# Kernel tuning notes

Measured on AMD Instinct MI355X. Metric: run time of the kernel, lower is better.

## Reference

```python
import jax, jax.numpy as jnp
import numpy as np

DIM = 100
SAMPLE_DS = 0.5
MAX_S = int(DIM / SAMPLE_DS) + 1  # 201, matches torch sample_ds_arr
DIRECTIONS = ['x', 'x', 'y', 'y']  # constant in the original forward


def _polygon_area(poly):
    # poly: [bs, num_v, 2]; shoelace-style area identical to torch loop
    y_max = jnp.max(poly[:, :, 1], axis=-1)            # [bs]
    x0 = poly[:, :, 0]; y0 = poly[:, :, 1]
    x1 = jnp.roll(x0, -1, axis=1); y1 = jnp.roll(y0, -1, axis=1)
    s = jnp.sum((x1 - x0) * (y_max[:, None] - (y1 + y0) * 0.5), axis=1)
    return jnp.abs(s)


def _line_sum(mask_m, x0, x1, y0, y1, axis_x):
    # mask_m: [bs, DIM, DIM]; x0,x1,y0,y1: [bs, num_v]
    # Vectorized version of torch get_samples + interpolated_sum:
    # masked_select/dedup are replaced by boolean keep masks (samples along an
    # edge are monotone, so the valid set is a contiguous run and "previous
    # compacted sample" == "previous step").
    steps = jnp.arange(MAX_S, dtype=mask_m.dtype)      # [S]
    vx = x1 - x0 + 1e-6
    vy = y1 - y0 + 1e-6
    n = jnp.sqrt(vx * vx + vy * vy)
    vx = vx / n; vy = vy / n
    xs = x0[..., None] + steps * vx[..., None]         # [bs, nv, S]
    ys = y0[..., None] + steps * vy[..., None]
    xlo = jnp.minimum(x0, x1)[..., None]; xhi = jnp.maximum(x0, x1)[..., None]
    ylo = jnp.minimum(y0, y1)[..., None]; yhi = jnp.maximum(y0, y1)[..., None]
    seg = ((xs <= xhi + 1e-3) & (xs >= xlo - 1e-3) &
           (ys <= yhi + 1e-3) & (ys >= ylo - 1e-3))
    u = xs if axis_x else ys
    bound = (u <= DIM - 1) & (u >= 0.0)
    valid = seg & bound
    # dedup on floor(u) along sample axis (torch get_uniques)
    fu = jnp.floor(u)
    prev_valid = jnp.pad(valid[..., :-1], ((0, 0), (0, 0), (1, 0)))
    prev_fu = jnp.pad(fu[..., :-1], ((0, 0), (0, 0), (1, 0)))
    first = valid & ~prev_valid
    keep = valid & (first | (fu != prev_fu))
    # bilinear interpolation (torch interpolated_sum)
    X0f = jnp.floor(xs); Y0f = jnp.floor(ys)
    w00 = (X0f + 1 - xs) * (Y0f + 1 - ys)
    w01 = (X0f + 1 - xs) * (ys - Y0f)
    w10 = (xs - X0f) * (Y0f + 1 - ys)
    w11 = (xs - X0f) * (ys - Y0f)
    Xi0 = jnp.clip(X0f, 0, DIM - 1).astype(jnp.int32)
    Xi1 = jnp.clip(X0f + 1, 0, DIM - 1).astype(jnp.int32)
    Yi0 = jnp.clip(Y0f, 0, DIM - 1).astype(jnp.int32)
    Yi1 = jnp.clip(Y0f + 1, 0, DIM - 1).astype(jnp.int32)
    gather = jax.vmap(lambda m, yy, xx: m[yy, xx])      # over batch
    val = (w00 * gather(mask_m, Yi0, Xi0) + w01 * gather(mask_m, Yi1, Xi0) +
           w10 * gather(mask_m, Yi0, Xi1) + w11 * gather(mask_m, Yi1, Xi1))
    return jnp.sum(jnp.where(keep, val, 0.0), axis=-1)  # [bs, nv]


def _polygon_area_mask(poly, gt_mask):
    # poly: [bs, nv, 2], gt_mask: [bs, 4, DIM, DIM]
    x0 = poly[:, :, 0]; y0 = poly[:, :, 1]
    x1 = jnp.roll(x0, -1, axis=1); y1 = jnp.roll(y0, -1, axis=1)
    ret = jnp.zeros(poly.shape[0], dtype=poly.dtype)
    for m, d in enumerate(DIRECTIONS):
        ax = (d == 'x')
        sign = jnp.where((x1 > x0) if ax else (y1 > y0), 1.0, -1.0)
        sf = _line_sum(gt_mask[:, m], x0, x1, y0, y1, ax)
        sb = _line_sum(gt_mask[:, m], x1, x0, y1, y0, ax)
        s = jnp.sum(sign * (sf + sb) * 0.5, axis=1)
        ret = ret + jnp.abs(s)
    return ret / len(DIRECTIONS)


def setup_inputs() -> dict:
    key = jax.random.key(0)
    k1, k2, k3 = jax.random.split(key, 3)
    bs, nv = 512, 64
    poly = jax.random.uniform(k1, (bs, nv, 2), dtype=jnp.float32) * (DIM - 1)
    gt = jax.random.uniform(k2, (bs, nv, 2), dtype=jnp.float32) * (DIM - 1)
    gt_mask = jax.random.uniform(k3, (bs, 4, DIM, DIM), dtype=jnp.float32)
    return {"poly": poly, "gt": gt, "gt_mask": gt_mask}


def reference(poly, gt, gt_mask):
    pred_area = _polygon_area(poly)
    gt_area = _polygon_area(gt)
    int_area = _polygon_area_mask(poly, gt_mask)
    union_area = pred_area + gt_area - int_area
    return int_area / union_area
```

## Files before the change

### kernel.cpp

```cpp
#include <hip/hip_runtime.h>
#include <math.h>

#define DIM   100
#define NV    64
#define BS    512
#define MAXCH 1792

template<bool AX>
__device__ __forceinline__ float mainloop(
    const unsigned char* smask, const float (*prm)[8],
    const unsigned short* chunkTab, int totE, int tid) {
  const int grp = tid >> 5;
  const int sub = (tid >> 3) & 3;
  const int st  = tid & 7;
  const int base0 = grp * 16 + sub * 4;
  float acc = 0.0f;

  for (int i = 0; i * 128 < totE; ++i) {
    const ushort4 ent = *reinterpret_cast<const ushort4*>(
        &chunkTab[i * 128 + base0]);

    #define SAMPLE(e) {                                                    \
      const int c = (e) >> 4;                                              \
      const float kf = (float)((((e) & 15) << 3) | st);                    \
      const float4 p = *reinterpret_cast<const float4*>(&prm[c][0]);       \
      const float4 q = *reinterpret_cast<const float4*>(&prm[c][4]);       \
      const float vu = AX ? p.z : p.w;                                     \
      const float u0 = AX ? p.x : p.y;                                     \
      const float fu0 = floorf(u0);                                        \
      const float ck = fu0 + ((vu > 0.0f) ? kf : -kf);                     \
      const float te = ceilf(fmaf(kf, q.z, q.w) - 0.005f);                 \
      const float u1 = __fadd_rn(__fmul_rn(te, vu), u0);                   \
      float t = (floorf(u1) == ck) ? te : (te + 1.0f);                     \
      t = fminf(fmaxf(t, 0.0f), 300.0f);                                   \
      const float xs = __fadd_rn(__fmul_rn(t, p.z), p.x);                  \
      const float ys = __fadd_rn(__fmul_rn(t, p.w), p.y);                  \
      const float X0 = floorf(xs), Y0 = floorf(ys);                        \
      const float wx1 = xs - X0, wy1 = ys - Y0;                            \
      const float wx0 = 1.0f - wx1, wy0 = 1.0f - wy1;                      \
      const int ix0 = (int)X0, iy0 = (int)Y0;                              \
      const int xi0 = min(max(ix0, 0), DIM - 1);                           \
      const int xi1 = min(max(ix0 + 1, 0), DIM - 1);                       \
      const int yi0 = min(max(iy0, 0), DIM - 1);                           \
      const int yi1 = min(max(iy0 + 1, 0), DIM - 1);                       \
      const int a00 = yi0 * DIM + xi0, a01 = yi1 * DIM + xi0;              \
      const int xoff = xi1 - xi0;                                          \
      const float g00 = (float)smask[a00];                                 \
      const float g01 = (float)smask[a01];                                 \
      const float g10 = (float)smask[a00 + xoff];                          \
      const float g11 = (float)smask[a01 + xoff];                          \
      const float val = wx0 * (wy0 * g00 + wy1 * g01) +                    \
                        wx1 * (wy0 * g10 + wy1 * g11);                     \
      const float w = (kf <= q.y) ? q.x : 0.0f;                            \
      acc = fmaf(w, val, acc);                                             \
    }
    SAMPLE(ent.x); SAMPLE(ent.y); SAMPLE(ent.z); SAMPLE(ent.w);
    #undef SAMPLE
  }
  return acc;
}

__global__ __launch_bounds__(256, 8) void diffiou_intersect(
    const float* __restrict__ poly, const float* __restrict__ gt_mask,
    float* __restrict__ ws) {
  __shared__ unsigned char smask[DIM * DIM];
  __shared__ float prm[128][8];
  __shared__ unsigned short chunkTab[MAXCH];
  __shared__ int   wsum[2];
  __shared__ int   totalChunks;
  __shared__ float red[4];

  const int bid = blockIdx.x;
  const int b   = bid >> 2;
  const int m   = bid & 3;
  const bool ax = (m < 2);
  const int tid = threadIdx.x;

  {
    const float4* src = reinterpret_cast<const float4*>(
        gt_mask + (size_t)(b * 4 + m) * (DIM * DIM));
    for (int j = tid; j < DIM * DIM / 4; j += 256) {
      const float4 v = src[j];
      uchar4 c;
      c.x = (unsigned char)__float2int_rn(v.x * 255.0f);
      c.y = (unsigned char)__float2int_rn(v.y * 255.0f);
      c.z = (unsigned char)__float2int_rn(v.z * 255.0f);
      c.w = (unsigned char)__float2int_rn(v.w * 255.0f);
      *reinterpret_cast<uchar4*>(&smask[j * 4]) = c;
    }
    for (int j = tid; j < MAXCH; j += 256) chunkTab[j] = 15;
  }

  int ncv = 0;
  if (tid < 128) {
    const int e  = tid >> 1;
    const int fb = tid & 1;
    const float* pb = poly + (size_t)b * NV * 2;
    const float ex0 = pb[e * 2 + 0], ey0 = pb[e * 2 + 1];
    const int   en  = (e + 1) & (NV - 1);
    const float ex1 = pb[en * 2 + 0], ey1 = pb[en * 2 + 1];
    const float sign = (ax ? (ex1 > ex0) : (ey1 > ey0)) ? 1.0f : -1.0f;
    const float x0 = fb ? ex1 : ex0, y0 = fb ? ey1 : ey0;
    const float x1 = fb ? ex0 : ex1, y1 = fb ? ey0 : ey1;
    float vx = (x1 - x0) + 1e-6f;
    float vy = (y1 - y0) + 1e-6f;
    const float n = __fsqrt_rn(__fadd_rn(__fmul_rn(vx, vx), __fmul_rn(vy, vy)));
    vx = __fdiv_rn(vx, n);
    vy = __fdiv_rn(vy, n);
    float xlo = fminf(x0, x1) - 0.001f, xhi = fmaxf(x0, x1) + 0.001f;
    float ylo = fminf(y0, y1) - 0.001f, yhi = fmaxf(y0, y1) + 0.001f;
    if (ax) { xlo = fmaxf(xlo, 0.0f); xhi = fminf(xhi, (float)(DIM - 1)); }
    else    { ylo = fmaxf(ylo, 0.0f); yhi = fminf(yhi, (float)(DIM - 1)); }

    #define VALID_AT(tt, out) {                                   \
      const float tf_ = (float)(tt);                              \
      const float xs_ = __fadd_rn(__fmul_rn(tf_, vx), x0);        \
      const float ys_ = __fadd_rn(__fmul_rn(tf_, vy), y0);        \
      out = (xs_ <= xhi) && (xs_ >= xlo) &&                       \
            (ys_ <= yhi) && (ys_ >= ylo);                         \
    }
    int T;
    bool v200; VALID_AT(200, v200);
    if (v200) { T = 200; }
    else {
      int lo = 0, hi = 200;
      #pragma unroll
      for (int it = 0; it < 8; ++it) {
        const int mid = (lo + hi) >> 1;
        bool vm; VALID_AT(mid, vm);
        if (vm) lo = mid; else hi = mid;
      }
      T = lo;
    }
    #undef VALID_AT

    const float vu  = ax ? vx : vy;
    const float u0  = ax ? x0 : y0;
    const float fu0 = floorf(u0);
    const float uT  = __fadd_rn(__fmul_rn((float)T, vu), u0);
    int K = abs((int)floorf(uT) - (int)fu0);
    K = min(K, 99);
    const float B = __fdiv_rn(1.0f, fabsf(vu));
    const float D = (vu > 0.0f) ? (fu0 - u0) : (u0 - fu0 - 1.0f);
    prm[tid][0] = x0;  prm[tid][1] = y0;
    prm[tid][2] = vx;  prm[tid][3] = vy;
    prm[tid][4] = sign * (0.5f / 255.0f);
    prm[tid][5] = (float)K;
    prm[tid][6] = B;
    prm[tid][7] = D * B;
    ncv = (K >> 3) + 1;
  }

  int v = ncv;
  #pragma unroll
  for (int i = 1; i < 64; i <<= 1) {
    const int w = __shfl_up(v, i, 64);
    if ((tid & 63) >= i) v += w;
  }
  if (((tid & 63) == 63) && (tid < 128)) wsum[tid >> 6] = v;
  __syncthreads();
  if ((tid >= 64) && (tid < 128)) v += wsum[0];
  if (tid < 128) {
    const int start = v - ncv;
    for (int k = 0; k < ncv; ++k)
      chunkTab[start + k] = (unsigned short)((tid << 4) | k);
    if (tid == 127) totalChunks = v;
  }
  __syncthreads();

  const int totE = totalChunks;
  const float acc = ax ? mainloop<true >(smask, prm, chunkTab, totE, tid)
                       : mainloop<false>(smask, prm, chunkTab, totE, tid);

  float a = acc;
  #pragma unroll
  for (int o = 32; o > 0; o >>= 1) a += __shfl_xor(a, o, 64);
  if ((tid & 63) == 0) red[tid >> 6] = a;
  __syncthreads();
  if (tid == 0) {
    const float s = red[0] + red[1] + red[2] + red[3];
    ws[bid] = fabsf(s);
  }
}

__device__ __forceinline__ float wave_area(const float* P, int b, int v) {
  const float x0 = P[(size_t)(b * NV + v) * 2 + 0];
  const float y0 = P[(size_t)(b * NV + v) * 2 + 1];
  const int vn = (v + 1) & (NV - 1);
  const float x1 = P[(size_t)(b * NV + vn) * 2 + 0];
  const float y1 = P[(size_t)(b * NV + vn) * 2 + 1];
  float ym = y0;
  #pragma unroll
  for (int o = 32; o > 0; o >>= 1) ym = fmaxf(ym, __shfl_xor(ym, o, 64));
  float term = (x1 - x0) * (ym - (y1 + y0) * 0.5f);
  #pragma unroll
  for (int o = 32; o > 0; o >>= 1) term += __shfl_xor(term, o, 64);
  return fabsf(term);
}

__global__ __launch_bounds__(64) void diffiou_finalize(
    const float* __restrict__ poly, const float* __restrict__ gt,
    const float* __restrict__ ws, float* __restrict__ out) {
  const int b = blockIdx.x;
  const int v = threadIdx.x;
  const float pa = wave_area(poly, b, v);
  const float ga = wave_area(gt, b, v);
  if (v == 0) {
    const float ia = 0.25f * (ws[b * 4 + 0] + ws[b * 4 + 1] +
                              ws[b * 4 + 2] + ws[b * 4 + 3]);
    out[b] = ia / (pa + ga - ia);
  }
}

extern "C" void kernel_launch(void* const* d_in, const int* in_sizes, int n_in,
                              void* d_out, int out_size, void* d_ws, size_t ws_size,
                              hipStream_t stream) {
  const float* poly    = (const float*)d_in[0];
  const float* gt      = (const float*)d_in[1];
  const float* gt_mask = (const float*)d_in[2];
  float* out = (float*)d_out;
  float* ws  = (float*)d_ws;

  hipLaunchKernelGGL(diffiou_intersect, dim3(BS * 4), dim3(256), 0, stream,
                     poly, gt_mask, ws);
  hipLaunchKernelGGL(diffiou_finalize, dim3(BS), dim3(64), 0, stream,
                     poly, gt, ws, out);
}
```

Measured before the change: 35.02 us.

## Pack horizontal pixel pairs in shared memory and shrink per-edge parameters

The mask is stored in LDS as 16-bit words holding each pixel and its right neighbour, with a padded column for the clamped edge. Each bilinear sample then needs two LDS reads instead of four. Per-edge parameters shrink from 8 floats to a float4 plus one meta float: sign and K are packed together, and B and D are recomputed per sample with a fast reciprocal. LDS use grows, so the occupancy hint drops from 8 to 6 blocks per CU, and the approximate reciprocal may change the computed sample step near boundaries.

```diff
diff --git a/kernel.cpp b/kernel.cpp
--- a/kernel.cpp
+++ b/kernel.cpp
@@ -4,11 +4,13 @@
 #define DIM   100
 #define NV    64
 #define BS    512
-#define MAXCH 1792
+#define MAXCH 1664
+#define PXW   104
+#define SHWC  (0.5f / 255.0f)
 
 template<bool AX>
 __device__ __forceinline__ float mainloop(
-    const unsigned char* smask, const float (*prm)[8],
+    const unsigned short* px, const float4* prmA, const float* meta,
     const unsigned short* chunkTab, int totE, int tid) {
   const int grp = tid >> 5;
   const int sub = (tid >> 3) & 3;
@@ -23,13 +25,15 @@
     #define SAMPLE(e) {                                                    \
       const int c = (e) >> 4;                                              \
       const float kf = (float)((((e) & 15) << 3) | st);                    \
-      const float4 p = *reinterpret_cast<const float4*>(&prm[c][0]);       \
-      const float4 q = *reinterpret_cast<const float4*>(&prm[c][4]);       \
+      const float4 p = prmA[c];                          \
+      const float mt = meta[c];                          \
       const float vu = AX ? p.z : p.w;                                     \
       const float u0 = AX ? p.x : p.y;                                     \
       const float fu0 = floorf(u0);                                        \
+      const float Bv = __builtin_amdgcn_rcpf(fabsf(vu));                   \
+      const float D  = (vu > 0.0f) ? (fu0 - u0) : (u0 - fu0 - 1.0f);       \
+      const float te = ceilf((kf + D) * Bv - 0.005f);                      \
       const float ck = fu0 + ((vu > 0.0f) ? kf : -kf);                     \
-      const float te = ceilf(fmaf(kf, q.z, q.w) - 0.005f);                 \
       const float u1 = __fadd_rn(__fmul_rn(te, vu), u0);                   \
       float t = (floorf(u1) == ck) ? te : (te + 1.0f);                     \
       t = fminf(fmaxf(t, 0.0f), 300.0f);                                   \
@@ -39,19 +43,18 @@
       const float wx1 = xs - X0, wy1 = ys - Y0;                            \
       const float wx0 = 1.0f - wx1, wy0 = 1.0f - wy1;                      \
       const int ix0 = (int)X0, iy0 = (int)Y0;                              \
-      const int xi0 = min(max(ix0, 0), DIM - 1);                           \
-      const int xi1 = min(max(ix0 + 1, 0), DIM - 1);                       \
+      const int ic  = min(max(ix0, -1), DIM - 1);                          \
+      const int ip  = (ic < 0) ? 100 : ic;                                 \
       const int yi0 = min(max(iy0, 0), DIM - 1);                           \
       const int yi1 = min(max(iy0 + 1, 0), DIM - 1);                       \
-      const int a00 = yi0 * DIM + xi0, a01 = yi1 * DIM + xi0;              \
-      const int xoff = xi1 - xi0;                                          \
-      const float g00 = (float)smask[a00];                                 \
-      const float g01 = (float)smask[a01];                                 \
-      const float g10 = (float)smask[a00 + xoff];                          \
-      const float g11 = (float)smask[a01 + xoff];                          \
-      const float val = wx0 * (wy0 * g00 + wy1 * g01) +                    \
-                        wx1 * (wy0 * g10 + wy1 * g11);                     \
-      const float w = (kf <= q.y) ? q.x : 0.0f;                            \
+      const unsigned int r0 = px[yi0 * PXW + ip];                          \
+      const unsigned int r1 = px[yi1 * PXW + ip];                          \
+      const float g00 = (float)(r0 & 255u), g10 = (float)(r0 >> 8);        \
+      const float g01 = (float)(r1 & 255u), g11 = (float)(r1 >> 8);        \
+      const float val = wy0 * (wx0 * g00 + wx1 * g10) +                    \
+                        wy1 * (wx0 * g01 + wx1 * g11);                     \
+      const float w = (kf < fabsf(mt)) ? __builtin_copysignf(SHWC, mt)     \
+                                       : 0.0f;                             \
       acc = fmaf(w, val, acc);                                             \
     }
     SAMPLE(ent.x); SAMPLE(ent.y); SAMPLE(ent.z); SAMPLE(ent.w);
@@ -60,11 +63,12 @@
   return acc;
 }
 
-__global__ __launch_bounds__(256, 8) void diffiou_intersect(
+__global__ __launch_bounds__(256, 6) void diffiou_intersect(
     const float* __restrict__ poly, const float* __restrict__ gt_mask,
     float* __restrict__ ws) {
-  __shared__ unsigned char smask[DIM * DIM];
-  __shared__ float prm[128][8];
+  __shared__ unsigned short px[DIM * PXW];
+  __shared__ float4 prmA[128];
+  __shared__ float  meta[128];
   __shared__ unsigned short chunkTab[MAXCH];
   __shared__ int   wsum[2];
   __shared__ int   totalChunks;
@@ -77,16 +81,27 @@
   const int tid = threadIdx.x;
 
   {
-    const float4* src = reinterpret_cast<const float4*>(
-        gt_mask + (size_t)(b * 4 + m) * (DIM * DIM));
-    for (int j = tid; j < DIM * DIM / 4; j += 256) {
-      const float4 v = src[j];
-      uchar4 c;
-      c.x = (unsigned char)__float2int_rn(v.x * 255.0f);
-      c.y = (unsigned char)__float2int_rn(v.y * 255.0f);
-      c.z = (unsigned char)__float2int_rn(v.z * 255.0f);
-      c.w = (unsigned char)__float2int_rn(v.w * 255.0f);
-      *reinterpret_cast<uchar4*>(&smask[j * 4]) = c;
+    const float* src = gt_mask + (size_t)(b * 4 + m) * (DIM * DIM);
+    for (int j = tid; j < 2500; j += 256) {
+      const int y = j / 25;
+      const int g = j - y * 25;
+      const float4 v = *reinterpret_cast<const float4*>(&src[y * DIM + 4 * g]);
+      const float v4 = src[y * DIM + min(4 * g + 4, DIM - 1)];
+      const int c0 = __float2int_rn(v.x * 255.0f);
+      const int c1 = __float2int_rn(v.y * 255.0f);
+      const int c2 = __float2int_rn(v.z * 255.0f);
+      const int c3 = __float2int_rn(v.w * 255.0f);
+      const int c4 = __float2int_rn(v4  * 255.0f);
+      ushort4 o;
+      o.x = (unsigned short)(c0 | (c1 << 8));
+      o.y = (unsigned short)(c1 | (c2 << 8));
+      o.z = (unsigned short)(c2 | (c3 << 8));
+      o.w = (unsigned short)(c3 | (c4 << 8));
+      *reinterpret_cast<ushort4*>(&px[y * PXW + 4 * g]) = o;
+    }
+    if (tid < DIM) {
+      const int c0 = __float2int_rn(src[tid * DIM] * 255.0f);
+      px[tid * PXW + 100] = (unsigned short)(c0 | (c0 << 8));
     }
     for (int j = tid; j < MAXCH; j += 256) chunkTab[j] = 15;
   }
@@ -140,14 +155,8 @@
     const float uT  = __fadd_rn(__fmul_rn((float)T, vu), u0);
     int K = abs((int)floorf(uT) - (int)fu0);
     K = min(K, 99);
-    const float B = __fdiv_rn(1.0f, fabsf(vu));
-    const float D = (vu > 0.0f) ? (fu0 - u0) : (u0 - fu0 - 1.0f);
-    prm[tid][0] = x0;  prm[tid][1] = y0;
-    prm[tid][2] = vx;  prm[tid][3] = vy;
-    prm[tid][4] = sign * (0.5f / 255.0f);
-    prm[tid][5] = (float)K;
-    prm[tid][6] = B;
-    prm[tid][7] = D * B;
+    prmA[tid] = make_float4(x0, y0, vx, vy);
+    meta[tid] = sign * ((float)K + 0.5f);
     ncv = (K >> 3) + 1;
   }
 
@@ -169,8 +178,8 @@
   __syncthreads();
 
   const int totE = totalChunks;
-  const float acc = ax ? mainloop<true >(smask, prm, chunkTab, totE, tid)
-                       : mainloop<false>(smask, prm, chunkTab, totE, tid);
+  const float acc = ax ? mainloop<true >(px, prmA, meta, chunkTab, totE, tid)
+                       : mainloop<false>(px, prmA, meta, chunkTab, totE, tid);
 
   float a = acc;
   #pragma unroll
```

New measurement: 40.91 us. +16.8%, slower.
